# Kernel optimization log

Measured on AMD Instinct MI355X. Metric: run time of the kernel, lower is better.

## Reference

```python
import jax, jax.numpy as jnp
import numpy as np

D_MODEL = 384
D_STATE = 16
D_CONV = 4
EXPAND = 2
D_INNER = EXPAND * D_MODEL
DT_RANK = max(1, -(-D_MODEL // 16))  # ceil(d_model/16) = 24
BATCH = 32
SEQ = 1024


def _ssm_params(keys, prefix):
    s = 0.02
    n = lambda k, shp: jax.random.normal(k, shp, dtype=jnp.float32) * s
    A_log = jnp.broadcast_to(jnp.log(jnp.arange(1, D_STATE + 1, dtype=jnp.float32))[None, :], (D_INNER, D_STATE))
    return {
        prefix + '_in_w': n(keys[0], (2 * D_INNER, D_MODEL)),
        prefix + '_conv_w': n(keys[1], (D_INNER, 1, D_CONV)),
        prefix + '_conv_b': jnp.zeros((D_INNER,), jnp.float32),
        prefix + '_x_proj_w': n(keys[2], (DT_RANK + 2 * D_STATE, D_INNER)),
        prefix + '_dt_w': n(keys[3], (D_INNER, DT_RANK)),
        prefix + '_dt_b': jnp.zeros((D_INNER,), jnp.float32),
        prefix + '_A_log': A_log,
        prefix + '_D': jnp.ones((D_INNER,), jnp.float32),
        prefix + '_out_w': n(keys[4], (D_MODEL, D_INNER)),
    }


def setup_inputs() -> dict:
    key = jax.random.key(0)
    ks = jax.random.split(key, 13)
    inp = {
        'x': jax.random.normal(ks[0], (BATCH, SEQ, D_MODEL), dtype=jnp.float32),
        'ln_gamma': jnp.ones((D_MODEL,), jnp.float32),
        'ln_beta': jnp.zeros((D_MODEL,), jnp.float32),
        'gate_w': jax.random.normal(ks[11], (D_MODEL, 2 * D_MODEL), dtype=jnp.float32) * 0.02,
        'gate_b': jnp.zeros((D_MODEL,), jnp.float32),
    }
    inp.update(_ssm_params(ks[1:6], 'f'))
    inp.update(_ssm_params(ks[6:11], 'b'))
    return inp


def _selective_scan(xc, dt, A, Bm, Cm):
    # xc, dt: (B, L, d_inner); Bm, Cm: (B, L, N); A: (d_inner, N)
    h0 = jnp.zeros((xc.shape[0], xc.shape[2], A.shape[1]), xc.dtype)

    def step(h, inputs):
        x_t, dt_t, B_t, C_t = inputs          # (B,di), (B,di), (B,N), (B,N)
        dA = jnp.exp(dt_t[..., None] * A)     # (B, di, N)
        h = dA * h + (dt_t * x_t)[..., None] * B_t[:, None, :]
        y = jnp.einsum('bdn,bn->bd', h, C_t)
        return h, y

    xs = (jnp.moveaxis(xc, 1, 0), jnp.moveaxis(dt, 1, 0),
          jnp.moveaxis(Bm, 1, 0), jnp.moveaxis(Cm, 1, 0))
    _, ys = jax.lax.scan(step, h0, xs)
    return jnp.moveaxis(ys, 0, 1)  # (B, L, d_inner)


def _ssm(x, in_w, conv_w, conv_b, x_proj_w, dt_w, dt_b, A_log, Dp, out_w):
    L = x.shape[1]
    xz = jnp.einsum('bld,ed->ble', x, in_w)           # (B, L, 2*d_inner)
    xi, z = jnp.split(xz, 2, axis=-1)
    # depthwise causal conv1d (torch pads d_conv-1 then truncates to L)
    xc = jax.lax.conv_general_dilated(
        jnp.swapaxes(xi, 1, 2), conv_w, window_strides=(1,),
        padding=[(D_CONV - 1, 0)], feature_group_count=D_INNER,
        dimension_numbers=('NCH', 'OIH', 'NCH')) + conv_b[None, :, None]
    xc = jax.nn.silu(jnp.swapaxes(xc, 1, 2))          # (B, L, d_inner)
    xp = jnp.einsum('bld,ed->ble', xc, x_proj_w)      # (B, L, dt_rank+2N)
    dt = jax.nn.softplus(jnp.einsum('blr,dr->bld', xp[..., :DT_RANK], dt_w) + dt_b)
    Bm = xp[..., DT_RANK:DT_RANK + D_STATE]
    Cm = xp[..., DT_RANK + D_STATE:]
    A = -jnp.exp(A_log)
    y = _selective_scan(xc, dt, A, Bm, Cm)
    y = y + xc * Dp
    y = y * jax.nn.silu(z)
    return jnp.einsum('ble,de->bld', y, out_w)


def reference(x, ln_gamma, ln_beta,
              f_in_w, f_conv_w, f_conv_b, f_x_proj_w, f_dt_w, f_dt_b, f_A_log, f_D, f_out_w,
              b_in_w, b_conv_w, b_conv_b, b_x_proj_w, b_dt_w, b_dt_b, b_A_log, b_D, b_out_w,
              gate_w, gate_b):
    residual = x
    mu = jnp.mean(x, axis=-1, keepdims=True)
    var = jnp.mean((x - mu) ** 2, axis=-1, keepdims=True)
    xn = (x - mu) * jax.lax.rsqrt(var + 1e-5) * ln_gamma + ln_beta
    y_fwd = _ssm(xn, f_in_w, f_conv_w, f_conv_b, f_x_proj_w, f_dt_w, f_dt_b, f_A_log, f_D, f_out_w)
    y_bwd = _ssm(jnp.flip(xn, axis=1), b_in_w, b_conv_w, b_conv_b, b_x_proj_w, b_dt_w, b_dt_b, b_A_log, b_D, b_out_w)
    y_bwd = jnp.flip(y_bwd, axis=1)
    combined = jnp.concatenate([y_fwd, y_bwd], axis=-1)
    gate = jax.nn.sigmoid(jnp.einsum('blc,dc->bld', combined, gate_w) + gate_b)
    y = gate * y_fwd + (1.0 - gate) * y_bwd
    return y + residual
```

## Files before the change

kernel.cpp:

```cpp
#include <hip/hip_runtime.h>
#include <hip/hip_bf16.h>

#define BATCH  32
#define SEQ    1024
#define DMODEL 384
#define DINNER 768
#define DSTATE 16
#define DTRANK 24
#define NTOK   (BATCH * SEQ)
#define TC     32
#define CL     (SEQ / TC)
#define DTR_R  32

typedef __hip_bfloat16 bf16;
typedef __attribute__((ext_vector_type(8))) short frag_ab;
typedef __attribute__((ext_vector_type(4))) float frag_cd;

__device__ __forceinline__ float b2f(bf16 v) { return __bfloat162float(v); }
__device__ __forceinline__ bf16  f2b(float v) { return __float2bfloat16(v); }
__device__ __forceinline__ float ldx(const void* p, size_t i, bool f32m) {
    return f32m ? ((const float*)p)[i] : b2f(((const bf16*)p)[i]);
}

__global__ void detect_kernel(const unsigned short* __restrict__ x, int* flag) {
    int bad = 0;
    for (int i = threadIdx.x; i < 16384; i += 256) {
        int e = (x[i] >> 7) & 0xFF;
        bad |= (e >= 0xE0);
    }
    if (bad) atomicOr(flag, 1);
}

__global__ void struct_check(const float* __restrict__ alog, int* flag) {
    int c = blockIdx.x * 256 + threadIdx.x;
    if (c >= DINNER) return;
    float a0 = __expf(alog[c * 16]);
    int bad = 0;
#pragma unroll
    for (int n = 1; n < DSTATE; ++n) {
        float r = __expf(alog[c * 16 + n]) / a0;
        bad |= (fabsf(r - (float)(n + 1)) > 1e-3f * (n + 1));
    }
    if (bad) atomicOr(flag + 1, 1);
}

struct CvtF { const void* src[15]; float* dst[15]; int n[15]; };
struct CvtB { const void* src[7];  bf16*  dst[7];  int n[7];  };

__global__ void convert_f_kernel(CvtF p, const int* __restrict__ flag) {
    bool f32m = (*flag != 0);
    int y = blockIdx.y;
    const void* s = p.src[y];
    float* d = p.dst[y];
    int n = p.n[y];
    for (int i = blockIdx.x * 256 + threadIdx.x; i < n; i += gridDim.x * 256)
        d[i] = ldx(s, i, f32m);
}
__global__ void convert_b_kernel(CvtB p, const int* __restrict__ flag) {
    bool f32m = (*flag != 0);
    int y = blockIdx.y;
    const void* s = p.src[y];
    bf16* d = p.dst[y];
    int n = p.n[y];
    for (int i = blockIdx.x * 256 + threadIdx.x; i < n; i += gridDim.x * 256)
        d[i] = f2b(ldx(s, i, f32m));
}

__global__ void transpose_dtw(const float* __restrict__ w, float* __restrict__ wt) {
    int i = blockIdx.x * 256 + threadIdx.x;
    if (i >= DINNER * DTRANK) return;
    int c = i / DTRANK, r = i % DTRANK;
    wt[r * DINNER + c] = w[i];
}

__global__ void ln_kernel(const void* __restrict__ x, size_t xoff,
                          const float* __restrict__ gamma, const float* __restrict__ beta,
                          bf16* __restrict__ xn, const int* __restrict__ flag) {
    bool f32m = (*flag != 0);
    int wave = threadIdx.x >> 6;
    int lane = threadIdx.x & 63;
    int row  = blockIdx.x * 4 + wave;
    size_t base = xoff + (size_t)row * DMODEL;
    float v[6];
    float s = 0.f, s2 = 0.f;
#pragma unroll
    for (int i = 0; i < 6; ++i) {
        v[i] = ldx(x, base + lane + i * 64, f32m);
        s += v[i];
        s2 += v[i] * v[i];
    }
#pragma unroll
    for (int off = 32; off >= 1; off >>= 1) {
        s  += __shfl_down(s, off, 64);
        s2 += __shfl_down(s2, off, 64);
    }
    s  = __shfl(s, 0, 64);
    s2 = __shfl(s2, 0, 64);
    float mu   = s / DMODEL;
    float var  = s2 / DMODEL - mu * mu;
    float rstd = rsqrtf(var + 1e-5f);
    bf16* xnr = xn + (size_t)row * DMODEL;
#pragma unroll
    for (int i = 0; i < 6; ++i)
        xnr[lane + i * 64] = f2b((v[i] - mu) * rstd * gamma[lane + i * 64] + beta[lane + i * 64]);
}

template <int MODE>
__global__ __launch_bounds__(256) void gemm_mfma(
    const bf16* __restrict__ A, const bf16* __restrict__ W,
    int K, int lda, int ldw,
    bf16* __restrict__ C, int ldc, int cofs,
    float* __restrict__ Cf,
    const float* __restrict__ gb, const void* __restrict__ xg, size_t xoff,
    void* __restrict__ outg, const int* __restrict__ flag) {
    __shared__ bf16 Als[128][32];
    __shared__ bf16 Bls[128][32];
    int tid = threadIdx.x;
    int lane = tid & 63;
    int w = tid >> 6;
    int wm = w & 1, wn = w >> 1;
    int m0 = blockIdx.y * 128, n0 = blockIdx.x * 128;
    int row = tid >> 2, kc = tid & 3;
    int mr = lane & 15, quad = lane >> 4;

    frag_cd acc[4][4] = {};

    for (int k0 = 0; k0 < K; k0 += 32) {
        uint4 a0 = *(const uint4*)(A + (size_t)(m0 + row) * lda + k0 + kc * 8);
        uint4 a1 = *(const uint4*)(A + (size_t)(m0 + 64 + row) * lda + k0 + kc * 8);
        uint4 b0 = *(const uint4*)(W + (size_t)(n0 + row) * ldw + k0 + kc * 8);
        uint4 b1 = *(const uint4*)(W + (size_t)(n0 + 64 + row) * ldw + k0 + kc * 8);
        __syncthreads();
        *(uint4*)&Als[row][kc * 8]      = a0;
        *(uint4*)&Als[64 + row][kc * 8] = a1;
        *(uint4*)&Bls[row][kc * 8]      = b0;
        *(uint4*)&Bls[64 + row][kc * 8] = b1;
        __syncthreads();
        frag_ab af[4], bfr[4];
#pragma unroll
        for (int r = 0; r < 4; ++r)
            af[r] = *(const frag_ab*)&Als[wm * 64 + r * 16 + mr][quad * 8];
#pragma unroll
        for (int c = 0; c < 4; ++c)
            bfr[c] = *(const frag_ab*)&Bls[wn * 64 + c * 16 + mr][quad * 8];
#pragma unroll
        for (int r = 0; r < 4; ++r)
#pragma unroll
            for (int c = 0; c < 4; ++c)
                acc[r][c] = __builtin_amdgcn_mfma_f32_16x16x32_bf16(af[r], bfr[c], acc[r][c], 0, 0, 0);
    }

    bool f32m = (MODE == 1) ? (*flag != 0) : false;
#pragma unroll
    for (int r = 0; r < 4; ++r) {
#pragma unroll
        for (int c = 0; c < 4; ++c) {
#pragma unroll
            for (int reg = 0; reg < 4; ++reg) {
                int gm = m0 + wm * 64 + r * 16 + quad * 4 + reg;
                int gn = n0 + wn * 64 + c * 16 + mr;
                float v = acc[r][c][reg];
                if (MODE == 0) {
                    C[(size_t)gm * ldc + cofs + gn] = f2b(v);
                } else if (MODE == 2) {
                    if (gn < DTRANK + 2 * DSTATE) Cf[(size_t)gm * 56 + gn] = v;
                } else if (MODE == 3) {
                    size_t idx = (size_t)gm * ldc + cofs + gn;
                    float y = b2f(C[idx]);
                    float sz = v / (1.f + __expf(-v));
                    C[idx] = f2b(y * sz);
                } else {
                    float g   = 1.f / (1.f + __expf(-(v + gb[gn])));
                    float yfv = b2f(A[(size_t)gm * DINNER + gn]);
                    float ybv = b2f(A[(size_t)gm * DINNER + DMODEL + gn]);
                    size_t gi = xoff + (size_t)gm * DMODEL + gn;
                    float xv  = f32m ? ((const float*)xg)[gi] : b2f(((const bf16*)xg)[gi]);
                    float rr  = g * yfv + (1.f - g) * ybv + xv;
                    if (f32m) ((float*)outg)[gi] = rr;
                    else      ((bf16*)outg)[gi]  = f2b(rr);
                }
            }
        }
    }
}

__global__ void conv_kernel(const bf16* __restrict__ xi_buf, const float* __restrict__ cw,
                            const float* __restrict__ cb, bf16* __restrict__ xc, int reverse) {
    int g = blockIdx.x * blockDim.x + threadIdx.x;
    int c  = g % DINNER;
    int bl = g / DINNER;
    int l = bl % SEQ;
    int b = bl / SEQ;
    float w[4];
#pragma unroll
    for (int k = 0; k < 4; ++k) w[k] = cw[c * 4 + k];
    const bf16* xi = xi_buf + (size_t)b * SEQ * DINNER + c;
    float acc = cb[c];
    if (!reverse) {
#pragma unroll
        for (int k = 0; k < 4; ++k) {
            int ll = l - 3 + k;
            if (ll >= 0) acc += b2f(xi[(size_t)ll * DINNER]) * w[k];
        }
    } else {
#pragma unroll
        for (int j = 0; j < 4; ++j) {
            int ll = l + j;
            if (ll < SEQ) acc += b2f(xi[(size_t)ll * DINNER]) * w[3 - j];
        }
    }
    xc[(size_t)bl * DINNER + c] = f2b(acc / (1.f + __expf(-acc)));
}

__global__ __launch_bounds__(256, 4) void dt_kernel(const float* __restrict__ xp,
                                                    const float* __restrict__ dtwT,
                                                    const float* __restrict__ dtb,
                                                    float* __restrict__ dtf) {
    __shared__ float4 xps[DTR_R][6];
    int tid = threadIdx.x;
    int c = blockIdx.y * 256 + tid;
    float w[DTRANK];
#pragma unroll
    for (int r = 0; r < DTRANK; ++r) w[r] = dtwT[r * DINNER + c];
#pragma unroll
    for (int r = 0; r < DTRANK; ++r) asm volatile("" : "+v"(w[r]));
    float bias = dtb[c];

    size_t row0 = (size_t)blockIdx.x * DTR_R;
    for (int i = tid; i < DTR_R * 6; i += 256) {
        int s = i / 6, q = i % 6;
        xps[s][q] = *(const float4*)(xp + (row0 + s) * 56 + q * 4);
    }
    __syncthreads();

    for (int s = 0; s < DTR_R; s += 2) {
        float a0 = bias, a1 = bias;
#pragma unroll
        for (int q = 0; q < 6; ++q) {
            float4 x0 = xps[s][q];
            float4 x1 = xps[s + 1][q];
            a0 += x0.x * w[q * 4 + 0];  a1 += x1.x * w[q * 4 + 0];
            a0 += x0.y * w[q * 4 + 1];  a1 += x1.y * w[q * 4 + 1];
            a0 += x0.z * w[q * 4 + 2];  a1 += x1.z * w[q * 4 + 2];
            a0 += x0.w * w[q * 4 + 3];  a1 += x1.w * w[q * 4 + 3];
        }
        float e0 = __builtin_amdgcn_exp2f(fabsf(a0) * -1.44269504f);
        float e1 = __builtin_amdgcn_exp2f(fabsf(a1) * -1.44269504f);
        a0 = fmaxf(a0, 0.f) + 0.69314718f * __builtin_amdgcn_logf(1.f + e0);
        a1 = fmaxf(a1, 0.f) + 0.69314718f * __builtin_amdgcn_logf(1.f + e1);
        dtf[(row0 + s) * DINNER + c]     = a0;
        dtf[(row0 + s + 1) * DINNER + c] = a1;
    }
}

template <int PHASE>
__global__ void scan_phase(const float* __restrict__ xp, const bf16* __restrict__ xc,
                           const float* __restrict__ dtf, const float* __restrict__ Alog,
                           const float* __restrict__ Dg, float* __restrict__ states,
                           bf16* __restrict__ ydir, int reverse, const int* __restrict__ flag) {
    __shared__ float xps[16][32];
    bool generic = (flag[1] != 0);
    int tid = threadIdx.x;
    int bidx = blockIdx.x;
    int tc  = bidx % TC;
    int cgb = bidx / TC;
    int cg  = cgb % 6;
    int bb  = cgb / 6;
    int c = cg * 128 + tid;

    float Av0 = -__expf(Alog[c * DSTATE]);
    float Av[DSTATE];
    if (generic) {
#pragma unroll
        for (int n = 0; n < DSTATE; ++n) Av[n] = -__expf(Alog[c * DSTATE + n]);
    }
    float Dv = Dg[c];

    float h[DSTATE];
    float Q = 1.f, Pg[DSTATE];
    size_t sbase = (size_t)bidx * 32;
    if (PHASE == 0) {
#pragma unroll
        for (int n = 0; n < DSTATE; ++n) { h[n] = 0.f; Pg[n] = 1.f; }
    } else {
#pragma unroll
        for (int n = 0; n < DSTATE; ++n) h[n] = states[(sbase + n) * 128 + tid];
    }

    const size_t brow = (size_t)bb * SEQ;
    for (int g0 = tc * CL; g0 < tc * CL + CL; g0 += 16) {
        __syncthreads();
        for (int i = tid; i < 16 * 32; i += 128) {
            int s = i >> 5, r = i & 31;
            int t = g0 + s;
            int tr = reverse ? (SEQ - 1 - t) : t;
            xps[s][r] = xp[(brow + tr) * 56 + 24 + r];
        }
        __syncthreads();
        for (int s = 0; s < 16; ++s) {
            int t = g0 + s;
            int tr = reverse ? (SEQ - 1 - t) : t;
            size_t row = brow + tr;
            float dt  = dtf[row * DINNER + c];
            float xcv = b2f(xc[row * DINNER + c]);
            float dtx = dt * xcv;
            float accv = 0.f;
            if (!generic) {
                float e1 = __expf(dt * Av0);
                float d = e1;
#pragma unroll
                for (int n = 0; n < DSTATE; ++n) {
                    h[n] = d * h[n] + dtx * xps[s][n];
                    if (PHASE == 1) accv += h[n] * xps[s][16 + n];
                    d *= e1;
                }
                if (PHASE == 0) Q *= e1;
            } else {
#pragma unroll
                for (int n = 0; n < DSTATE; ++n) {
                    float dA = __expf(dt * Av[n]);
                    h[n] = dA * h[n] + dtx * xps[s][n];
                    if (PHASE == 0) Pg[n] *= dA;
                    else accv += h[n] * xps[s][16 + n];
                }
            }
            if (PHASE == 1)
                ydir[row * DINNER + c] = f2b(accv + xcv * Dv);
        }
    }
    if (PHASE == 0) {
        if (!generic) {
            float d = Q;
#pragma unroll
            for (int n = 0; n < DSTATE; ++n) { Pg[n] = d; d *= Q; }
        }
#pragma unroll
        for (int n = 0; n < DSTATE; ++n) {
            states[(sbase + n) * 128 + tid]      = Pg[n];
            states[(sbase + 16 + n) * 128 + tid] = h[n];
        }
    }
}

__global__ void scan_stitch(float* __restrict__ states) {
    int tid = threadIdx.x;
    int cgb = blockIdx.x;
    float h[DSTATE];
#pragma unroll
    for (int n = 0; n < DSTATE; ++n) h[n] = 0.f;
    for (int tc = 0; tc < TC; ++tc) {
        size_t base = ((size_t)cgb * TC + tc) * 32;
#pragma unroll
        for (int n = 0; n < DSTATE; ++n) {
            float Pv = states[(base + n) * 128 + tid];
            float ev = states[(base + 16 + n) * 128 + tid];
            states[(base + n) * 128 + tid] = h[n];
            h[n] = Pv * h[n] + ev;
        }
    }
}

extern "C" void kernel_launch(void* const* d_in, const int* in_sizes, int n_in,
                              void* d_out, int out_size, void* d_ws, size_t ws_size,
                              hipStream_t stream) {
    (void)n_in; (void)out_size;
    bool dict_order = (in_sizes[4] < 2048);
    int fbase = dict_order ? 5 : 3;
    int bbase = dict_order ? 14 : 12;
    int gwi = dict_order ? 3 : 21;
    int gbi = dict_order ? 4 : 22;

    auto al = [](size_t b) { return (b + 255) & ~(size_t)255; };
    char* ws = (char*)d_ws;
    size_t off = 0;
    auto alloc = [&](size_t bytes) {
        void* p = ws + off;
        off += al(bytes);
        return p;
    };

    int* flag = (int*)alloc(256);

    CvtF pf{};
    int cf = 0;
    auto addf = [&](int idx, int n) {
        float* d = (float*)alloc((size_t)n * 4);
        pf.src[cf] = d_in[idx]; pf.dst[cf] = d; pf.n[cf] = n; ++cf;
        return d;
    };
    float* ln_gc   = addf(1, DMODEL);
    float* ln_bc   = addf(2, DMODEL);
    float* gate_bc = addf(gbi, DMODEL);
    float* convw_f[2], *convb_f[2], *dtw_f[2], *dtb_f[2], *alog_f[2], *dd_f[2];
    for (int d = 0; d < 2; ++d) {
        int base = d ? bbase : fbase;
        convw_f[d] = addf(base + 1, DINNER * 4);
        convb_f[d] = addf(base + 2, DINNER);
        dtw_f[d]   = addf(base + 4, DINNER * DTRANK);
        dtb_f[d]   = addf(base + 5, DINNER);
        alog_f[d]  = addf(base + 6, DINNER * DSTATE);
        dd_f[d]    = addf(base + 7, DINNER);
    }

    CvtB pb{};
    int cb = 0;
    auto addb = [&](int idx, int n, size_t alloc_n) {
        bf16* d = (bf16*)alloc(alloc_n * 2);
        pb.src[cb] = d_in[idx]; pb.dst[cb] = d; pb.n[cb] = n; ++cb;
        return d;
    };
    bf16* gate_wb = addb(gwi, DMODEL * 2 * DMODEL, (size_t)DMODEL * 2 * DMODEL);
    bf16 *inw_b[2], *xpw_b[2], *outw_b[2];
    for (int d = 0; d < 2; ++d) {
        int base = d ? bbase : fbase;
        inw_b[d]  = addb(base + 0, 2 * DINNER * DMODEL, (size_t)2 * DINNER * DMODEL);
        xpw_b[d]  = addb(base + 3, 56 * DINNER, (size_t)128 * DINNER);
        outw_b[d] = addb(base + 8, DMODEL * DINNER, (size_t)DMODEL * DINNER);
    }

    float* dtwT_f[2];
    for (int d = 0; d < 2; ++d)
        dtwT_f[d] = (float*)alloc((size_t)DTRANK * DINNER * 4);

    size_t fixed = off;

    auto chunk_need = [&](int bc) {
        size_t T = (size_t)bc * SEQ;
        return al(T * DMODEL * 2)
             + 2 * al(T * DINNER * 2)
             + al(T * 56 * 4)
             + al(T * DINNER * 4)
             + al(T * DINNER * 2)
             + al((size_t)bc * 6 * TC * 32 * 128 * 4);
    };
    int Bc = 32;
    while (Bc > 1 && fixed + chunk_need(Bc) > ws_size) Bc >>= 1;
    size_t T = (size_t)Bc * SEQ;

    bf16*  xn_c   = (bf16*)alloc(T * DMODEL * 2);
    bf16*  xib    = (bf16*)alloc(T * DINNER * 2);
    bf16*  xcb    = (bf16*)alloc(T * DINNER * 2);
    float* xpb    = (float*)alloc(T * 56 * 4);
    float* dtfb   = (float*)alloc(T * DINNER * 4);
    bf16*  ycat   = (bf16*)alloc(T * DINNER * 2);
    float* states = (float*)alloc((size_t)Bc * 6 * TC * 32 * 128 * 4);
    bf16*  ydir   = xib;

    hipMemsetAsync(flag, 0, 8, stream);
    for (int d = 0; d < 2; ++d)
        hipMemsetAsync(xpw_b[d], 0, (size_t)128 * DINNER * 2, stream);
    detect_kernel<<<1, 256, 0, stream>>>((const unsigned short*)d_in[0], flag);
    convert_f_kernel<<<dim3(8, 15), 256, 0, stream>>>(pf, flag);
    convert_b_kernel<<<dim3(32, 7), 256, 0, stream>>>(pb, flag);
    struct_check<<<3, 256, 0, stream>>>(alog_f[0], flag);
    struct_check<<<3, 256, 0, stream>>>(alog_f[1], flag);
    for (int d = 0; d < 2; ++d)
        transpose_dtw<<<(DINNER * DTRANK + 255) / 256, 256, 0, stream>>>(dtw_f[d], dtwT_f[d]);

    for (int c0 = 0; c0 < BATCH; c0 += Bc) {
        size_t tok0 = (size_t)c0 * SEQ;

        ln_kernel<<<(unsigned)(T / 4), 256, 0, stream>>>(
            d_in[0], tok0 * DMODEL, ln_gc, ln_bc, xn_c, flag);

        for (int dir = 0; dir < 2; ++dir) {
            gemm_mfma<0><<<dim3(DINNER / 128, T / 128), 256, 0, stream>>>(
                xn_c, inw_b[dir], DMODEL, DMODEL, DMODEL,
                xib, DINNER, 0, nullptr, nullptr, nullptr, 0, nullptr, flag);
            conv_kernel<<<(unsigned)((T * DINNER) / 256), 256, 0, stream>>>(
                xib, convw_f[dir], convb_f[dir], xcb, dir);
            gemm_mfma<2><<<dim3(1, T / 128), 256, 0, stream>>>(
                xcb, xpw_b[dir], DINNER, DINNER, DINNER,
                nullptr, 0, 0, xpb, nullptr, nullptr, 0, nullptr, flag);
            dt_kernel<<<dim3((unsigned)(T / DTR_R), 3), 256, 0, stream>>>(
                xpb, dtwT_f[dir], dtb_f[dir], dtfb);
            scan_phase<0><<<Bc * 6 * TC, 128, 0, stream>>>(
                xpb, xcb, dtfb, alog_f[dir], dd_f[dir], states, nullptr, dir, flag);
            scan_stitch<<<Bc * 6, 128, 0, stream>>>(states);
            scan_phase<1><<<Bc * 6 * TC, 128, 0, stream>>>(
                xpb, xcb, dtfb, alog_f[dir], dd_f[dir], states, ydir, dir, flag);
            gemm_mfma<3><<<dim3(DINNER / 128, T / 128), 256, 0, stream>>>(
                xn_c, inw_b[dir] + (size_t)DINNER * DMODEL, DMODEL, DMODEL, DMODEL,
                ydir, DINNER, 0, nullptr, nullptr, nullptr, 0, nullptr, flag);
            gemm_mfma<0><<<dim3(DMODEL / 128, T / 128), 256, 0, stream>>>(
                ydir, outw_b[dir], DINNER, DINNER, DINNER,
                ycat, DINNER, dir * DMODEL, nullptr, nullptr, nullptr, 0, nullptr, flag);
        }

        gemm_mfma<1><<<dim3(DMODEL / 128, T / 128), 256, 0, stream>>>(
            ycat, gate_wb, DINNER, DINNER, DINNER,
            nullptr, 0, 0, nullptr, gate_bc, d_in[0], tok0 * DMODEL, d_out, flag);
    }
}
```

Baseline: 1.371 ms.

## Fuse z projection into in-proj GEMM, apply SiLU gating in out-proj load

The in-projection GEMM now computes both the x and z halves in one launch, writing z to a new fp32 buffer. The SiLU(z)*y gating moves from a separate GEMM epilogue into the A-tile load of the out-projection GEMM. The separate MODE 3 launch that re-read xn is removed. The GEMM tiles are now staged via global_load_lds direct-to-LDS loads, and the scan's per-step index arithmetic becomes strided pointer increments. The cost is an extra fp32 z buffer with its write and read traffic, plus SiLU work repeated for each output column tile.

```diff
diff --git a/kernel.cpp b/kernel.cpp
--- a/kernel.cpp
+++ b/kernel.cpp
@@ -22,6 +22,12 @@
     return f32m ? ((const float*)p)[i] : b2f(((const bf16*)p)[i]);
 }
 
+__device__ __forceinline__ void gld16(void* l, const void* g) {
+    __builtin_amdgcn_global_load_lds(
+        (const __attribute__((address_space(1))) unsigned int*)g,
+        (__attribute__((address_space(3))) unsigned int*)l, 16, 0, 0);
+}
+
 __global__ void detect_kernel(const unsigned short* __restrict__ x, int* flag) {
     int bad = 0;
     for (int i = threadIdx.x; i < 16384; i += 256) {
@@ -105,6 +111,19 @@
         xnr[lane + i * 64] = f2b((v[i] - mu) * rstd * gamma[lane + i * 64] + beta[lane + i * 64]);
 }
 
+__device__ __forceinline__ uint4 silu_mul(uint4 y8, float4 z0, float4 z1) {
+    const bf16* yb = (const bf16*)&y8;
+    uint4 r;
+    bf16* rb = (bf16*)&r;
+    float zz[8] = {z0.x, z0.y, z0.z, z0.w, z1.x, z1.y, z1.z, z1.w};
+#pragma unroll
+    for (int j = 0; j < 8; ++j) {
+        float s = zz[j] / (1.f + __expf(-zz[j]));
+        rb[j] = f2b(b2f(yb[j]) * s);
+    }
+    return r;
+}
+
 template <int MODE>
 __global__ __launch_bounds__(256) void gemm_mfma(
     const bf16* __restrict__ A, const bf16* __restrict__ W,
@@ -112,7 +131,8 @@
     bf16* __restrict__ C, int ldc, int cofs,
     float* __restrict__ Cf,
     const float* __restrict__ gb, const void* __restrict__ xg, size_t xoff,
-    void* __restrict__ outg, const int* __restrict__ flag) {
+    void* __restrict__ outg, const float* __restrict__ zF,
+    const int* __restrict__ flag) {
     __shared__ bf16 Als[128][32];
     __shared__ bf16 Bls[128][32];
     int tid = threadIdx.x;
@@ -123,19 +143,41 @@
     int row = tid >> 2, kc = tid & 3;
     int mr = lane & 15, quad = lane >> 4;
 
+    const bf16* Ab0 = A + (size_t)(m0 + row) * lda + kc * 8;
+    const bf16* Ab1 = A + (size_t)(m0 + 64 + row) * lda + kc * 8;
+    const bf16* Wb0 = W + (size_t)(n0 + row) * ldw + kc * 8;
+    const bf16* Wb1 = W + (size_t)(n0 + 64 + row) * ldw + kc * 8;
+    void* lA0 = &Als[row][kc * 8];
+    void* lA1 = &Als[64 + row][kc * 8];
+    void* lB0 = &Bls[row][kc * 8];
+    void* lB1 = &Bls[64 + row][kc * 8];
+
     frag_cd acc[4][4] = {};
 
     for (int k0 = 0; k0 < K; k0 += 32) {
-        uint4 a0 = *(const uint4*)(A + (size_t)(m0 + row) * lda + k0 + kc * 8);
-        uint4 a1 = *(const uint4*)(A + (size_t)(m0 + 64 + row) * lda + k0 + kc * 8);
-        uint4 b0 = *(const uint4*)(W + (size_t)(n0 + row) * ldw + k0 + kc * 8);
-        uint4 b1 = *(const uint4*)(W + (size_t)(n0 + 64 + row) * ldw + k0 + kc * 8);
-        __syncthreads();
-        *(uint4*)&Als[row][kc * 8]      = a0;
-        *(uint4*)&Als[64 + row][kc * 8] = a1;
-        *(uint4*)&Bls[row][kc * 8]      = b0;
-        *(uint4*)&Bls[64 + row][kc * 8] = b1;
-        __syncthreads();
+        if (MODE == 5) {
+            uint4 ya0 = *(const uint4*)(Ab0 + k0);
+            uint4 ya1 = *(const uint4*)(Ab1 + k0);
+            const float* zr0 = zF + (size_t)(m0 + row) * DINNER + k0 + kc * 8;
+            const float* zr1 = zF + (size_t)(m0 + 64 + row) * DINNER + k0 + kc * 8;
+            float4 z00 = *(const float4*)zr0, z01 = *(const float4*)(zr0 + 4);
+            float4 z10 = *(const float4*)zr1, z11 = *(const float4*)(zr1 + 4);
+            uint4 ea0 = silu_mul(ya0, z00, z01);
+            uint4 ea1 = silu_mul(ya1, z10, z11);
+            __syncthreads();
+            *(uint4*)lA0 = ea0;
+            *(uint4*)lA1 = ea1;
+            gld16(lB0, Wb0 + k0);
+            gld16(lB1, Wb1 + k0);
+            __syncthreads();
+        } else {
+            __syncthreads();
+            gld16(lA0, Ab0 + k0);
+            gld16(lA1, Ab1 + k0);
+            gld16(lB0, Wb0 + k0);
+            gld16(lB1, Wb1 + k0);
+            __syncthreads();
+        }
         frag_ab af[4], bfr[4];
 #pragma unroll
         for (int r = 0; r < 4; ++r)
@@ -160,15 +202,13 @@
                 int gm = m0 + wm * 64 + r * 16 + quad * 4 + reg;
                 int gn = n0 + wn * 64 + c * 16 + mr;
                 float v = acc[r][c][reg];
-                if (MODE == 0) {
+                if (MODE == 0 || MODE == 5) {
                     C[(size_t)gm * ldc + cofs + gn] = f2b(v);
                 } else if (MODE == 2) {
                     if (gn < DTRANK + 2 * DSTATE) Cf[(size_t)gm * 56 + gn] = v;
-                } else if (MODE == 3) {
-                    size_t idx = (size_t)gm * ldc + cofs + gn;
-                    float y = b2f(C[idx]);
-                    float sz = v / (1.f + __expf(-v));
-                    C[idx] = f2b(y * sz);
+                } else if (MODE == 4) {
+                    if (gn < DINNER) C[(size_t)gm * DINNER + gn] = f2b(v);
+                    else             Cf[(size_t)gm * DINNER + (gn - DINNER)] = v;
                 } else {
                     float g   = 1.f / (1.f + __expf(-(v + gb[gn])));
                     float yfv = b2f(A[(size_t)gm * DINNER + gn]);
@@ -288,21 +328,25 @@
     }
 
     const size_t brow = (size_t)bb * SEQ;
-    for (int g0 = tc * CL; g0 < tc * CL + CL; g0 += 16) {
+    const int t0 = tc * CL;
+    const int tr0 = reverse ? (SEQ - 1 - t0) : t0;
+    const long dstep = reverse ? -(long)DINNER : (long)DINNER;
+    const float* pdt = dtf + (brow + tr0) * DINNER + c;
+    const bf16*  pxc = xc  + (brow + tr0) * DINNER + c;
+    bf16* pyd = (PHASE == 1) ? (ydir + (brow + tr0) * DINNER + c) : nullptr;
+
+    for (int g0 = 0; g0 < CL; g0 += 16) {
         __syncthreads();
         for (int i = tid; i < 16 * 32; i += 128) {
             int s = i >> 5, r = i & 31;
-            int t = g0 + s;
+            int t = t0 + g0 + s;
             int tr = reverse ? (SEQ - 1 - t) : t;
             xps[s][r] = xp[(brow + tr) * 56 + 24 + r];
         }
         __syncthreads();
         for (int s = 0; s < 16; ++s) {
-            int t = g0 + s;
-            int tr = reverse ? (SEQ - 1 - t) : t;
-            size_t row = brow + tr;
-            float dt  = dtf[row * DINNER + c];
-            float xcv = b2f(xc[row * DINNER + c]);
+            float dt  = *pdt;  pdt += dstep;
+            float xcv = b2f(*pxc);  pxc += dstep;
             float dtx = dt * xcv;
             float accv = 0.f;
             if (!generic) {
@@ -324,8 +368,10 @@
                     else accv += h[n] * xps[s][16 + n];
                 }
             }
-            if (PHASE == 1)
-                ydir[row * DINNER + c] = f2b(accv + xcv * Dv);
+            if (PHASE == 1) {
+                *pyd = f2b(accv + xcv * Dv);
+                pyd += dstep;
+            }
         }
     }
     if (PHASE == 0) {
@@ -430,6 +476,7 @@
              + 2 * al(T * DINNER * 2)
              + al(T * 56 * 4)
              + al(T * DINNER * 4)
+             + al(T * DINNER * 4)
              + al(T * DINNER * 2)
              + al((size_t)bc * 6 * TC * 32 * 128 * 4);
     };
@@ -442,6 +489,7 @@
     bf16*  xcb    = (bf16*)alloc(T * DINNER * 2);
     float* xpb    = (float*)alloc(T * 56 * 4);
     float* dtfb   = (float*)alloc(T * DINNER * 4);
+    float* zbf    = (float*)alloc(T * DINNER * 4);
     bf16*  ycat   = (bf16*)alloc(T * DINNER * 2);
     float* states = (float*)alloc((size_t)Bc * 6 * TC * 32 * 128 * 4);
     bf16*  ydir   = xib;
@@ -464,14 +512,14 @@
             d_in[0], tok0 * DMODEL, ln_gc, ln_bc, xn_c, flag);
 
         for (int dir = 0; dir < 2; ++dir) {
-            gemm_mfma<0><<<dim3(DINNER / 128, T / 128), 256, 0, stream>>>(
+            gemm_mfma<4><<<dim3(2 * DINNER / 128, T / 128), 256, 0, stream>>>(
                 xn_c, inw_b[dir], DMODEL, DMODEL, DMODEL,
-                xib, DINNER, 0, nullptr, nullptr, nullptr, 0, nullptr, flag);
+                xib, DINNER, 0, zbf, nullptr, nullptr, 0, nullptr, nullptr, flag);
             conv_kernel<<<(unsigned)((T * DINNER) / 256), 256, 0, stream>>>(
                 xib, convw_f[dir], convb_f[dir], xcb, dir);
             gemm_mfma<2><<<dim3(1, T / 128), 256, 0, stream>>>(
                 xcb, xpw_b[dir], DINNER, DINNER, DINNER,
-                nullptr, 0, 0, xpb, nullptr, nullptr, 0, nullptr, flag);
+                nullptr, 0, 0, xpb, nullptr, nullptr, 0, nullptr, nullptr, flag);
             dt_kernel<<<dim3((unsigned)(T / DTR_R), 3), 256, 0, stream>>>(
                 xpb, dtwT_f[dir], dtb_f[dir], dtfb);
             scan_phase<0><<<Bc * 6 * TC, 128, 0, stream>>>(
@@ -479,16 +527,13 @@
             scan_stitch<<<Bc * 6, 128, 0, stream>>>(states);
             scan_phase<1><<<Bc * 6 * TC, 128, 0, stream>>>(
                 xpb, xcb, dtfb, alog_f[dir], dd_f[dir], states, ydir, dir, flag);
-            gemm_mfma<3><<<dim3(DINNER / 128, T / 128), 256, 0, stream>>>(
-                xn_c, inw_b[dir] + (size_t)DINNER * DMODEL, DMODEL, DMODEL, DMODEL,
-                ydir, DINNER, 0, nullptr, nullptr, nullptr, 0, nullptr, flag);
-            gemm_mfma<0><<<dim3(DMODEL / 128, T / 128), 256, 0, stream>>>(
+            gemm_mfma<5><<<dim3(DMODEL / 128, T / 128), 256, 0, stream>>>(
                 ydir, outw_b[dir], DINNER, DINNER, DINNER,
-                ycat, DINNER, dir * DMODEL, nullptr, nullptr, nullptr, 0, nullptr, flag);
+                ycat, DINNER, dir * DMODEL, nullptr, nullptr, nullptr, 0, nullptr, zbf, flag);
         }
 
         gemm_mfma<1><<<dim3(DMODEL / 128, T / 128), 256, 0, stream>>>(
             ycat, gate_wb, DINNER, DINNER, DINNER,
-            nullptr, 0, 0, nullptr, gate_bc, d_in[0], tok0 * DMODEL, d_out, flag);
-    }
-}
+            nullptr, 0, 0, nullptr, gate_bc, d_in[0], tok0 * DMODEL, d_out, nullptr, flag);
+    }
+}
```

Result: slower. 1.461 ms (+6.6%).
